# Optimization experiments

Hardware: AMD Instinct MI355X
Metric: run time of the kernel (lower is better)

The kernel has to match this reference:

```python
import jax, jax.numpy as jnp
import numpy as np

D_MODEL = 1024
NUM_HEADS = 16
D_K = D_MODEL // NUM_HEADS
BATCH = 4
SEQ = 2048


def setup_inputs() -> dict:
    key = jax.random.key(0)
    ks = jax.random.split(key, 12)
    s = 0.02
    inp = {
        "Q": jax.random.normal(ks[0], (BATCH, SEQ, D_MODEL), jnp.float32),
        "K": jax.random.normal(ks[1], (BATCH, SEQ, D_MODEL), jnp.float32),
        "V": jax.random.normal(ks[2], (BATCH, SEQ, D_MODEL), jnp.float32),
        "mask": jnp.tril(jnp.ones((SEQ, SEQ), jnp.int32)),  # causal: 0 = masked
        "Wq": jax.random.normal(ks[3], (D_MODEL, D_MODEL), jnp.float32) * s,
        "bq": jax.random.normal(ks[4], (D_MODEL,), jnp.float32) * s,
        "Wk": jax.random.normal(ks[5], (D_MODEL, D_MODEL), jnp.float32) * s,
        "bk": jax.random.normal(ks[6], (D_MODEL,), jnp.float32) * s,
        "Wv": jax.random.normal(ks[7], (D_MODEL, D_MODEL), jnp.float32) * s,
        "bv": jax.random.normal(ks[8], (D_MODEL,), jnp.float32) * s,
        "Wo": jax.random.normal(ks[9], (D_MODEL, D_MODEL), jnp.float32) * s,
        "bo": jax.random.normal(ks[10], (D_MODEL,), jnp.float32) * s,
    }
    return inp


def _split_heads(x):
    # (b, s, d_model) -> (b, h, s, d_k)
    b, s, _ = x.shape
    return x.reshape(b, s, NUM_HEADS, D_K).transpose(0, 2, 1, 3)


def reference(Q, K, V, mask, Wq, bq, Wk, bk, Wv, bv, Wo, bo):
    # Linear projections (torch Linear: x @ W^T + b)
    q = _split_heads(Q @ Wq.T + bq)  # (b, h, s, dk)
    k = _split_heads(K @ Wk.T + bk)
    v = _split_heads(V @ Wv.T + bv)
    scale = 1.0 / jnp.sqrt(jnp.asarray(D_K, q.dtype))
    scores = jnp.einsum("bhqd,bhkd->bhqk", q, k) * scale  # (b, h, s, s)
    scores = jnp.where(mask == 0, jnp.asarray(-jnp.inf, scores.dtype), scores)
    attn = jax.nn.softmax(scores, axis=-1)
    out = jnp.einsum("bhqk,bhkd->bhqd", attn, v)  # (b, h, s, dk)
    b, h, s, dk = out.shape
    out = out.transpose(0, 2, 1, 3).reshape(b, s, h * dk)  # combine heads
    return out @ Wo.T + bo
```

## Files before the change

### kernel.cpp

```cpp
#include <hip/hip_runtime.h>


typedef _Float16 f16;
typedef _Float16 f16x8 __attribute__((ext_vector_type(8)));
typedef _Float16 f16x4 __attribute__((ext_vector_type(4)));
typedef float floatx4 __attribute__((ext_vector_type(4)));
typedef float f32x16 __attribute__((ext_vector_type(16)));
typedef unsigned int uint4v __attribute__((ext_vector_type(4)));
typedef unsigned short u16x8 __attribute__((ext_vector_type(8)));

#define SEQ 2048
#define DM 1024
#define NH 16
#define DK 64
#define MR 8192

#define QSCALE 0.18033688011112042f

#if __has_builtin(__builtin_amdgcn_exp2f)
#define EXP2(x) __builtin_amdgcn_exp2f(x)
#else
#define EXP2(x) __expf(0.6931471805599453f * (x))
#endif

__device__ __forceinline__ void gl_lds16(const void* g, void* lds) {
    __builtin_amdgcn_global_load_lds(
        (const __attribute__((address_space(1))) unsigned int*)g,
        (__attribute__((address_space(3))) unsigned int*)lds,
        16, 0, 0);
}

__device__ __forceinline__ unsigned short cvt_rne_u16(float x) {
    unsigned int r;
    asm("v_cvt_f16_f32 %0, %1" : "=v"(r) : "v"(x));
    return (unsigned short)r;
}

struct ConvArgs {
    const float* s[4];
    f16* d[4];
};

__global__ __launch_bounds__(256) void convk(ConvArgs a) {
    int bx = blockIdx.x;
    int t = bx >> 10, base = bx & 1023;
    int i = base * 256 + threadIdx.x;
    float4 v = ((const float4*)a.s[t])[i];
    f16x4 o;
    o.x = (f16)v.x; o.y = (f16)v.y; o.z = (f16)v.z; o.w = (f16)v.w;
    ((f16x4*)a.d[t])[i] = o;
}

template <int MODE, bool AF32>
__device__ __forceinline__ void gemm_body(
    const void* __restrict__ Ap, const f16* __restrict__ W,
    const float* __restrict__ bias, void* __restrict__ outp,
    int m0, int n0, float oscale, void* As_raw, f16* Bs)
{
    const int tid = threadIdx.x;
    const int wave = tid >> 6, lane = tid & 63;
    const int quad = lane >> 4, ln = lane & 15;
    const int wr = wave >> 1, wc = wave & 1;

    floatx4 acc[4][4] = {};

    for (int kt = 0; kt < 16; ++kt) {
        const int k0 = kt * 64;
        if constexpr (AF32) {
            const float* Af = (const float*)Ap;
#pragma unroll
            for (int s = 0; s < 8; ++s) {
                int c = s * 256 + tid;
                int row = c >> 4, lc = (c & 15) ^ (row & 15);
                gl_lds16(Af + (size_t)(m0 + row) * 1024 + k0 + lc * 4,
                         (char*)As_raw + (s * 256 + wave * 64) * 16);
            }
        } else {
            const f16* Ah = (const f16*)Ap;
#pragma unroll
            for (int s = 0; s < 4; ++s) {
                int c = s * 256 + tid;
                int row = c >> 3, lc = (c & 7) ^ (row & 7);
                gl_lds16(Ah + (size_t)(m0 + row) * 1024 + k0 + lc * 8,
                         (char*)As_raw + (s * 256 + wave * 64) * 16);
            }
        }
#pragma unroll
        for (int s = 0; s < 4; ++s) {
            int c = s * 256 + tid;
            int row = c >> 3, lc = (c & 7) ^ (row & 7);
            gl_lds16(W + (size_t)(n0 + row) * 1024 + k0 + lc * 8,
                     (char*)Bs + (s * 256 + wave * 64) * 16);
        }
        __syncthreads();
#pragma unroll
        for (int kk = 0; kk < 64; kk += 32) {
            const int cb = kk >> 3;
            f16x8 af[4], bf[4];
#pragma unroll
            for (int i = 0; i < 4; ++i) {
                int row = wr * 64 + i * 16 + ln;
                if constexpr (AF32) {
                    const float* Asf = (const float*)As_raw;
                    const int j = cb + quad;
                    const int p0 = (2 * j) ^ ln;
                    const int p1 = (2 * j + 1) ^ ln;
                    floatx4 lo = *(const floatx4*)&Asf[row * 64 + p0 * 4];
                    floatx4 hi = *(const floatx4*)&Asf[row * 64 + p1 * 4];
                    u16x8 u;
                    u[0] = cvt_rne_u16(lo[0]); u[1] = cvt_rne_u16(lo[1]);
                    u[2] = cvt_rne_u16(lo[2]); u[3] = cvt_rne_u16(lo[3]);
                    u[4] = cvt_rne_u16(hi[0]); u[5] = cvt_rne_u16(hi[1]);
                    u[6] = cvt_rne_u16(hi[2]); u[7] = cvt_rne_u16(hi[3]);
                    af[i] = __builtin_bit_cast(f16x8, u);
                } else {
                    const f16* Ash = (const f16*)As_raw;
                    af[i] = *(const f16x8*)&Ash[row * 64 + (((cb + quad) ^ (ln & 7)) << 3)];
                }
            }
#pragma unroll
            for (int j = 0; j < 4; ++j) {
                int row = wc * 64 + j * 16 + ln;
                bf[j] = *(const f16x8*)&Bs[row * 64 + (((cb + quad) ^ (ln & 7)) << 3)];
            }
#pragma unroll
            for (int i = 0; i < 4; ++i)
#pragma unroll
                for (int j = 0; j < 4; ++j)
                    acc[i][j] = __builtin_amdgcn_mfma_f32_16x16x32_f16(
                        af[i], bf[j], acc[i][j], 0, 0, 0);
        }
        __syncthreads();
    }

#pragma unroll
    for (int i = 0; i < 4; ++i) {
#pragma unroll
        for (int j = 0; j < 4; ++j) {
            int col = n0 + wc * 64 + j * 16 + ln;
            float bc = bias[col];
            int rowb = m0 + wr * 64 + i * 16 + quad * 4;
            if (MODE == 1) {
                int bb = rowb >> 11, ss = rowb & 2047;
                int hh = col >> 6, dd = col & 63;
                f16x4 o4;
#pragma unroll
                for (int r = 0; r < 4; ++r)
                    o4[r] = (f16)((acc[i][j][r] + bc) * oscale);
                *(f16x4*)&((f16*)outp)[(((size_t)(bb * 16 + hh)) * 64 + dd) * 2048 + ss] = o4;
            } else {
#pragma unroll
                for (int r = 0; r < 4; ++r) {
                    float v = (acc[i][j][r] + bc) * oscale;
                    int rm = rowb + r;
                    if (MODE == 2) {
                        ((float*)outp)[(size_t)rm * 1024 + col] = v;
                    } else {
                        int bb = rm >> 11, ss = rm & 2047;
                        int hh = col >> 6, dd = col & 63;
                        ((f16*)outp)[(((size_t)(bb * 16 + hh)) * 2048 + ss) * 64 + dd] = (f16)v;
                    }
                }
            }
        }
    }
}

struct G3Args {
    const float* A[3]; const f16* W[3]; const float* b[3]; f16* o[3];
};

__global__ __launch_bounds__(256, 2) void gemm_qkv(G3Args g) {
    __shared__ alignas(16) float Asf[128 * 64];
    __shared__ alignas(16) f16 Bs[128 * 64];
    const int z = blockIdx.z;
    const int m0 = blockIdx.x * 128, n0 = blockIdx.y * 128;
    if (z < 2)
        gemm_body<0, true>(g.A[z], g.W[z], g.b[z], g.o[z], m0, n0,
                           z == 0 ? QSCALE : 1.0f, Asf, Bs);
    else
        gemm_body<1, true>(g.A[2], g.W[2], g.b[2], g.o[2], m0, n0, 1.0f, Asf, Bs);
}

__global__ __launch_bounds__(256, 2) void gemm_out(
    const f16* __restrict__ A, const f16* __restrict__ W,
    const float* __restrict__ bias, float* __restrict__ outp)
{
    __shared__ alignas(16) f16 As[128 * 64];
    __shared__ alignas(16) f16 Bs[128 * 64];
    gemm_body<2, false>(A, W, bias, outp, blockIdx.x * 128, blockIdx.y * 128,
                        1.0f, As, Bs);
}

__global__ __launch_bounds__(256, 3) void attn_kernel(
    const f16* __restrict__ Qp, const f16* __restrict__ Kp,
    const f16* __restrict__ Vt, f16* __restrict__ Op)
{
    __shared__ alignas(16) f16 ks[128 * 64];
    __shared__ alignas(16) f16 vs[64 * 128];

    const int tid = threadIdx.x;
    const int wave = tid >> 6, lane = tid & 63;
    const int h = lane >> 5, c31 = lane & 31;
    const int bh = blockIdx.x;
    const f16* qb = Qp + (size_t)bh * SEQ * DK;
    const f16* kbp = Kp + (size_t)bh * SEQ * DK;
    const f16* vb = Vt + (size_t)bh * DK * SEQ;
    const int b = bh >> 4, hd = bh & 15;

    f16x8 ones;
#pragma unroll
    for (int e = 0; e < 8; ++e) ones[e] = (f16)1.0f;

    for (int half = 0; half < 2; ++half) {
        const int jt = half ? (15 - blockIdx.y) : blockIdx.y;
        const int q0 = jt * 128;

#pragma unroll
        for (int s = 0; s < 4; ++s) {
            int c = s * 256 + tid;
            int row = c >> 3, lc = (c & 7) ^ (row & 7);
            gl_lds16(qb + (size_t)(q0 + row) * 64 + lc * 8,
                     (char*)ks + (s * 256 + wave * 64) * 16);
        }
        __syncthreads();
        f16x8 bq[4];
#pragma unroll
        for (int t = 0; t < 4; ++t) {
            int row = wave * 32 + c31;
            bq[t] = *(const f16x8*)&ks[row * 64 + (((2 * t + h) ^ (row & 7)) << 3)];
        }
        __syncthreads();

        f32x16 oacc0 = {}, oacc1 = {}, lacc = {};

        const int nk = jt + 1;
        for (int kt = 0; kt < nk; ++kt) {
            const int k0 = kt * 128;
#pragma unroll
            for (int s = 0; s < 4; ++s) {
                int c = s * 256 + tid;
                int row = c >> 3, lc = (c & 7) ^ (row & 7);
                gl_lds16(kbp + (size_t)(k0 + row) * 64 + lc * 8,
                         (char*)ks + (s * 256 + wave * 64) * 16);
            }
#pragma unroll
            for (int s = 0; s < 4; ++s) {
                int c = s * 256 + tid;
                int row = c >> 4, lc = (c & 15) ^ (row & 15);
                gl_lds16(vb + (size_t)row * SEQ + k0 + lc * 8,
                         (char*)vs + (s * 256 + wave * 64) * 16);
            }
            __syncthreads();

            const bool diag = (kt == jt);
            const int qloc = wave * 32 + c31;

#pragma unroll
            for (int kb = 0; kb < 4; ++kb) {
                f32x16 sacc = {};
#pragma unroll
                for (int t = 0; t < 4; ++t) {
                    int row = kb * 32 + c31;
                    f16x8 ak = *(const f16x8*)&ks[row * 64 + (((2 * t + h) ^ (row & 7)) << 3)];
                    sacc = __builtin_amdgcn_mfma_f32_32x32x16_f16(
                        ak, bq[t], sacc, 0, 0, 0);
                }

                unsigned pg[4][2];
#pragma unroll
                for (int g = 0; g < 4; ++g) {
#pragma unroll
                    for (int j = 0; j < 2; ++j) {
                        const int r = 4 * g + 2 * j;
                        const int kg = kb * 32 + 8 * g + 4 * h + 2 * j;
                        float s0 = sacc[r], s1 = sacc[r + 1];
                        float p0 = (diag && kg > qloc) ? 0.0f : EXP2(s0);
                        float p1 = (diag && kg + 1 > qloc) ? 0.0f : EXP2(s1);
                        auto pp = __builtin_amdgcn_cvt_pkrtz(p0, p1);
                        pg[g][j] = __builtin_bit_cast(unsigned, pp);
                    }
                }

#pragma unroll
                for (int sub = 0; sub < 2; ++sub) {
                    const int s = 2 * kb + sub;
                    unsigned a0 = pg[2 * sub][0], a1 = pg[2 * sub][1];
                    unsigned b0 = pg[2 * sub + 1][0], b1 = pg[2 * sub + 1][1];
                    asm("v_permlane32_swap_b32 %0, %1" : "+v"(a0), "+v"(b0));
                    asm("v_permlane32_swap_b32 %0, %1" : "+v"(a1), "+v"(b1));
                    uint4v fw;
                    fw.x = a0; fw.y = a1; fw.z = b0; fw.w = b1;
                    f16x8 F = __builtin_bit_cast(f16x8, fw);

                    lacc = __builtin_amdgcn_mfma_f32_32x32x16_f16(
                        F, ones, lacc, 0, 0, 0);
                    {
                        int row = c31;
                        f16x8 bv = *(const f16x8*)&vs[row * 128 + (((2 * s + h) ^ (row & 15)) << 3)];
                        oacc0 = __builtin_amdgcn_mfma_f32_32x32x16_f16(
                            F, bv, oacc0, 0, 0, 0);
                    }
                    {
                        int row = 32 + c31;
                        f16x8 bv = *(const f16x8*)&vs[row * 128 + (((2 * s + h) ^ (row & 15)) << 3)];
                        oacc1 = __builtin_amdgcn_mfma_f32_32x32x16_f16(
                            F, bv, oacc1, 0, 0, 0);
                    }
                }
            }
            __syncthreads();
        }

#pragma unroll
        for (int r = 0; r < 16; ++r) {
            const int qr = (r & 3) + 8 * (r >> 2) + 4 * h;
            const int rowg = q0 + wave * 32 + qr;
            float inv = 1.0f / lacc[r];
            {
                int col = hd * 64 + c31;
                Op[((size_t)b * SEQ + rowg) * DM + col] = (f16)(oacc0[r] * inv);
            }
            {
                int col = hd * 64 + 32 + c31;
                Op[((size_t)b * SEQ + rowg) * DM + col] = (f16)(oacc1[r] * inv);
            }
        }
    }
}

extern "C" void kernel_launch(void* const* d_in, const int* in_sizes, int n_in,
                              void* d_out, int out_size, void* d_ws, size_t ws_size,
                              hipStream_t stream) {
    const float* Q  = (const float*)d_in[0];
    const float* K  = (const float*)d_in[1];
    const float* V  = (const float*)d_in[2];
    const float* Wq = (const float*)d_in[4];
    const float* bq = (const float*)d_in[5];
    const float* Wk = (const float*)d_in[6];
    const float* bk = (const float*)d_in[7];
    const float* Wv = (const float*)d_in[8];
    const float* bv = (const float*)d_in[9];
    const float* Wo = (const float*)d_in[10];
    const float* bo = (const float*)d_in[11];

    char* ws = (char*)d_ws;
    f16* Wqb = (f16*)ws;
    f16* Wkb = Wqb + (size_t)DM * DM;
    f16* Wvb = Wkb + (size_t)DM * DM;
    f16* Wob = Wvb + (size_t)DM * DM;
    f16* qp  = Wob + (size_t)DM * DM;
    f16* kp  = qp + (size_t)MR * DM;
    f16* vtp = kp + (size_t)MR * DM;
    f16* Ao  = vtp + (size_t)MR * DM;

    ConvArgs ca;
    ca.s[0] = Wq; ca.d[0] = Wqb;
    ca.s[1] = Wk; ca.d[1] = Wkb;
    ca.s[2] = Wv; ca.d[2] = Wvb;
    ca.s[3] = Wo; ca.d[3] = Wob;
    convk<<<4 * 1024, 256, 0, stream>>>(ca);

    G3Args g;
    g.A[0] = Q; g.W[0] = Wqb; g.b[0] = bq; g.o[0] = qp;
    g.A[1] = K; g.W[1] = Wkb; g.b[1] = bk; g.o[1] = kp;
    g.A[2] = V; g.W[2] = Wvb; g.b[2] = bv; g.o[2] = vtp;
    gemm_qkv<<<dim3(64, 8, 3), 256, 0, stream>>>(g);

    attn_kernel<<<dim3(64, 8), 256, 0, stream>>>(qp, kp, vtp, Ao);

    gemm_out<<<dim3(64, 8), 256, 0, stream>>>(Ao, Wob, bo, (float*)d_out);
}
```

Before: 304.8 us.

## Load fp32 A operand directly to registers in QKV GEMM, drop A LDS tile

```diff
diff --git a/kernel.cpp b/kernel.cpp
--- a/kernel.cpp
+++ b/kernel.cpp
@@ -51,40 +51,20 @@
     ((f16x4*)a.d[t])[i] = o;
 }
 
-template <int MODE, bool AF32>
-__device__ __forceinline__ void gemm_body(
-    const void* __restrict__ Ap, const f16* __restrict__ W,
-    const float* __restrict__ bias, void* __restrict__ outp,
-    int m0, int n0, float oscale, void* As_raw, f16* Bs)
+template <int MODE>
+__device__ __forceinline__ void gemm_f32a_body(
+    const float* __restrict__ A, const f16* __restrict__ W,
+    const float* __restrict__ bias, f16* __restrict__ outp,
+    int m0, int n0, float oscale, f16* Bs)
 {
     const int tid = threadIdx.x;
     const int wave = tid >> 6, lane = tid & 63;
     const int quad = lane >> 4, ln = lane & 15;
-    const int wr = wave >> 1, wc = wave & 1;
-
-    floatx4 acc[4][4] = {};
+
+    floatx4 acc[2][8] = {};
 
     for (int kt = 0; kt < 16; ++kt) {
         const int k0 = kt * 64;
-        if constexpr (AF32) {
-            const float* Af = (const float*)Ap;
-#pragma unroll
-            for (int s = 0; s < 8; ++s) {
-                int c = s * 256 + tid;
-                int row = c >> 4, lc = (c & 15) ^ (row & 15);
-                gl_lds16(Af + (size_t)(m0 + row) * 1024 + k0 + lc * 4,
-                         (char*)As_raw + (s * 256 + wave * 64) * 16);
-            }
-        } else {
-            const f16* Ah = (const f16*)Ap;
-#pragma unroll
-            for (int s = 0; s < 4; ++s) {
-                int c = s * 256 + tid;
-                int row = c >> 3, lc = (c & 7) ^ (row & 7);
-                gl_lds16(Ah + (size_t)(m0 + row) * 1024 + k0 + lc * 8,
-                         (char*)As_raw + (s * 256 + wave * 64) * 16);
-            }
-        }
 #pragma unroll
         for (int s = 0; s < 4; ++s) {
             int c = s * 256 + tid;
@@ -92,54 +72,52 @@
             gl_lds16(W + (size_t)(n0 + row) * 1024 + k0 + lc * 8,
                      (char*)Bs + (s * 256 + wave * 64) * 16);
         }
-        __syncthreads();
-#pragma unroll
-        for (int kk = 0; kk < 64; kk += 32) {
-            const int cb = kk >> 3;
-            f16x8 af[4], bf[4];
-#pragma unroll
-            for (int i = 0; i < 4; ++i) {
-                int row = wr * 64 + i * 16 + ln;
-                if constexpr (AF32) {
-                    const float* Asf = (const float*)As_raw;
-                    const int j = cb + quad;
-                    const int p0 = (2 * j) ^ ln;
-                    const int p1 = (2 * j + 1) ^ ln;
-                    floatx4 lo = *(const floatx4*)&Asf[row * 64 + p0 * 4];
-                    floatx4 hi = *(const floatx4*)&Asf[row * 64 + p1 * 4];
-                    u16x8 u;
-                    u[0] = cvt_rne_u16(lo[0]); u[1] = cvt_rne_u16(lo[1]);
-                    u[2] = cvt_rne_u16(lo[2]); u[3] = cvt_rne_u16(lo[3]);
-                    u[4] = cvt_rne_u16(hi[0]); u[5] = cvt_rne_u16(hi[1]);
-                    u[6] = cvt_rne_u16(hi[2]); u[7] = cvt_rne_u16(hi[3]);
-                    af[i] = __builtin_bit_cast(f16x8, u);
-                } else {
-                    const f16* Ash = (const f16*)As_raw;
-                    af[i] = *(const f16x8*)&Ash[row * 64 + (((cb + quad) ^ (ln & 7)) << 3)];
-                }
-            }
-#pragma unroll
-            for (int j = 0; j < 4; ++j) {
-                int row = wc * 64 + j * 16 + ln;
-                bf[j] = *(const f16x8*)&Bs[row * 64 + (((cb + quad) ^ (ln & 7)) << 3)];
-            }
-#pragma unroll
-            for (int i = 0; i < 4; ++i)
-#pragma unroll
-                for (int j = 0; j < 4; ++j)
+        float4 av[4][2];
+#pragma unroll
+        for (int f = 0; f < 4; ++f) {
+            const int i = f & 1, kk01 = f >> 1;
+            const int row = wave * 32 + i * 16 + ln;
+            const float* src =
+                A + (size_t)(m0 + row) * 1024 + k0 + (kk01 * 4 + quad) * 8;
+            av[f][0] = *(const float4*)src;
+            av[f][1] = *(const float4*)(src + 4);
+        }
+        __syncthreads();
+#pragma unroll
+        for (int kk01 = 0; kk01 < 2; ++kk01) {
+            const int cb = kk01 * 4;
+            f16x8 af[2];
+#pragma unroll
+            for (int i = 0; i < 2; ++i) {
+                const float4 lo = av[kk01 * 2 + i][0];
+                const float4 hi = av[kk01 * 2 + i][1];
+                u16x8 u;
+                u[0] = cvt_rne_u16(lo.x); u[1] = cvt_rne_u16(lo.y);
+                u[2] = cvt_rne_u16(lo.z); u[3] = cvt_rne_u16(lo.w);
+                u[4] = cvt_rne_u16(hi.x); u[5] = cvt_rne_u16(hi.y);
+                u[6] = cvt_rne_u16(hi.z); u[7] = cvt_rne_u16(hi.w);
+                af[i] = __builtin_bit_cast(f16x8, u);
+            }
+#pragma unroll
+            for (int j = 0; j < 8; ++j) {
+                int row = j * 16 + ln;
+                f16x8 bf = *(const f16x8*)&Bs[row * 64 + (((cb + quad) ^ (ln & 7)) << 3)];
+#pragma unroll
+                for (int i = 0; i < 2; ++i)
                     acc[i][j] = __builtin_amdgcn_mfma_f32_16x16x32_f16(
-                        af[i], bf[j], acc[i][j], 0, 0, 0);
+                        af[i], bf, acc[i][j], 0, 0, 0);
+            }
         }
         __syncthreads();
     }
 
 #pragma unroll
-    for (int i = 0; i < 4; ++i) {
-#pragma unroll
-        for (int j = 0; j < 4; ++j) {
-            int col = n0 + wc * 64 + j * 16 + ln;
+    for (int i = 0; i < 2; ++i) {
+#pragma unroll
+        for (int j = 0; j < 8; ++j) {
+            int col = n0 + j * 16 + ln;
             float bc = bias[col];
-            int rowb = m0 + wr * 64 + i * 16 + quad * 4;
+            int rowb = m0 + wave * 32 + i * 16 + quad * 4;
             if (MODE == 1) {
                 int bb = rowb >> 11, ss = rowb & 2047;
                 int hh = col >> 6, dd = col & 63;
@@ -147,19 +125,15 @@
 #pragma unroll
                 for (int r = 0; r < 4; ++r)
                     o4[r] = (f16)((acc[i][j][r] + bc) * oscale);
-                *(f16x4*)&((f16*)outp)[(((size_t)(bb * 16 + hh)) * 64 + dd) * 2048 + ss] = o4;
+                *(f16x4*)&outp[(((size_t)(bb * 16 + hh)) * 64 + dd) * 2048 + ss] = o4;
             } else {
 #pragma unroll
                 for (int r = 0; r < 4; ++r) {
                     float v = (acc[i][j][r] + bc) * oscale;
                     int rm = rowb + r;
-                    if (MODE == 2) {
-                        ((float*)outp)[(size_t)rm * 1024 + col] = v;
-                    } else {
-                        int bb = rm >> 11, ss = rm & 2047;
-                        int hh = col >> 6, dd = col & 63;
-                        ((f16*)outp)[(((size_t)(bb * 16 + hh)) * 2048 + ss) * 64 + dd] = (f16)v;
-                    }
+                    int bb = rm >> 11, ss = rm & 2047;
+                    int hh = col >> 6, dd = col & 63;
+                    outp[(((size_t)(bb * 16 + hh)) * 2048 + ss) * 64 + dd] = (f16)v;
                 }
             }
         }
@@ -171,15 +145,14 @@
 };
 
 __global__ __launch_bounds__(256, 2) void gemm_qkv(G3Args g) {
-    __shared__ alignas(16) float Asf[128 * 64];
     __shared__ alignas(16) f16 Bs[128 * 64];
     const int z = blockIdx.z;
     const int m0 = blockIdx.x * 128, n0 = blockIdx.y * 128;
     if (z < 2)
-        gemm_body<0, true>(g.A[z], g.W[z], g.b[z], g.o[z], m0, n0,
-                           z == 0 ? QSCALE : 1.0f, Asf, Bs);
+        gemm_f32a_body<0>(g.A[z], g.W[z], g.b[z], g.o[z], m0, n0,
+                          z == 0 ? QSCALE : 1.0f, Bs);
     else
-        gemm_body<1, true>(g.A[2], g.W[2], g.b[2], g.o[2], m0, n0, 1.0f, Asf, Bs);
+        gemm_f32a_body<1>(g.A[2], g.W[2], g.b[2], g.o[2], m0, n0, 1.0f, Bs);
 }
 
 __global__ __launch_bounds__(256, 2) void gemm_out(
@@ -188,8 +161,71 @@
 {
     __shared__ alignas(16) f16 As[128 * 64];
     __shared__ alignas(16) f16 Bs[128 * 64];
-    gemm_body<2, false>(A, W, bias, outp, blockIdx.x * 128, blockIdx.y * 128,
-                        1.0f, As, Bs);
+    const int m0 = blockIdx.x * 128, n0 = blockIdx.y * 128;
+
+    const int tid = threadIdx.x;
+    const int wave = tid >> 6, lane = tid & 63;
+    const int quad = lane >> 4, ln = lane & 15;
+    const int wr = wave >> 1, wc = wave & 1;
+
+    floatx4 acc[4][4] = {};
+
+    for (int kt = 0; kt < 16; ++kt) {
+        const int k0 = kt * 64;
+#pragma unroll
+        for (int s = 0; s < 4; ++s) {
+            int c = s * 256 + tid;
+            int row = c >> 3, lc = (c & 7) ^ (row & 7);
+            gl_lds16(A + (size_t)(m0 + row) * 1024 + k0 + lc * 8,
+                     (char*)As + (s * 256 + wave * 64) * 16);
+        }
+#pragma unroll
+        for (int s = 0; s < 4; ++s) {
+            int c = s * 256 + tid;
+            int row = c >> 3, lc = (c & 7) ^ (row & 7);
+            gl_lds16(W + (size_t)(n0 + row) * 1024 + k0 + lc * 8,
+                     (char*)Bs + (s * 256 + wave * 64) * 16);
+        }
+        __syncthreads();
+#pragma unroll
+        for (int kk = 0; kk < 64; kk += 32) {
+            const int cb = kk >> 3;
+            f16x8 af[4], bf[4];
+#pragma unroll
+            for (int i = 0; i < 4; ++i) {
+                int row = wr * 64 + i * 16 + ln;
+                af[i] = *(const f16x8*)&As[row * 64 + (((cb + quad) ^ (ln & 7)) << 3)];
+            }
+#pragma unroll
+            for (int j = 0; j < 4; ++j) {
+                int row = wc * 64 + j * 16 + ln;
+                bf[j] = *(const f16x8*)&Bs[row * 64 + (((cb + quad) ^ (ln & 7)) << 3)];
+            }
+#pragma unroll
+            for (int i = 0; i < 4; ++i)
+#pragma unroll
+                for (int j = 0; j < 4; ++j)
+                    acc[i][j] = __builtin_amdgcn_mfma_f32_16x16x32_f16(
+                        af[i], bf[j], acc[i][j], 0, 0, 0);
+        }
+        __syncthreads();
+    }
+
+#pragma unroll
+    for (int i = 0; i < 4; ++i) {
+#pragma unroll
+        for (int j = 0; j < 4; ++j) {
+            int col = n0 + wc * 64 + j * 16 + ln;
+            float bc = bias[col];
+            int rowb = m0 + wr * 64 + i * 16 + quad * 4;
+#pragma unroll
+            for (int r = 0; r < 4; ++r) {
+                float v = acc[i][j][r] + bc;
+                int rm = rowb + r;
+                outp[(size_t)rm * 1024 + col] = v;
+            }
+        }
+    }
 }
 
 __global__ __launch_bounds__(256, 3) void attn_kernel(
```

After: 356.0 us. 16.8% more time.
